# Kernel tuning notes

Hardware: AMD Instinct MI355X
Metric: run time of the kernel (lower is better)

## Reference

```python
import jax, jax.numpy as jnp
import numpy as np

T, B, D, H, L = 512, 64, 1024, 1024, 2
W_SCALE = 0.02  # keep tanh out of saturation


def setup_inputs() -> dict:
    key = jax.random.key(0)
    ks = jax.random.split(key, 7)
    return {
        "x": jax.random.normal(ks[0], (T, B, D), dtype=jnp.float32),
        "Wi": jax.random.normal(ks[1], (L, H, D), dtype=jnp.float32) * W_SCALE,
        "bi": jax.random.normal(ks[2], (L, H), dtype=jnp.float32) * W_SCALE,
        "Wh": jax.random.normal(ks[3], (L, H, H), dtype=jnp.float32) * W_SCALE,
        "bh": jax.random.normal(ks[4], (L, H), dtype=jnp.float32) * W_SCALE,
        "Wo": jax.random.normal(ks[5], (L, H, H), dtype=jnp.float32) * W_SCALE,
        "bo": jax.random.normal(ks[6], (L, H), dtype=jnp.float32) * W_SCALE,
    }


def reference(x, Wi, bi, Wh, bh, Wo, bo):
    # Faithful to the original: ONE hidden state shared across all layers,
    # overwritten by each RNNCell call within a timestep.
    num_layers = Wi.shape[0]
    batch = x.shape[1]
    hidden0 = jnp.zeros((batch, Wh.shape[-1]), dtype=x.dtype)

    def step(hidden, xt):
        out = xt
        for l in range(num_layers):
            # h = i2h(out) + h2h(hidden); o = h2o(h); new hidden = tanh(h)
            h = out @ Wi[l].T + bi[l] + hidden @ Wh[l].T + bh[l]  # [B,H]
            out = h @ Wo[l].T + bo[l]
            hidden = jnp.tanh(h)
        return hidden, out

    final_hidden, outs = jax.lax.scan(step, hidden0, x)  # outs: [T,B,H]
    return outs, final_hidden
```

## Files before the change

### kernel.cpp

```cpp
#include <hip/hip_runtime.h>
#include <cstdint>
#include <cstddef>

#define TT   512
#define NWG  256
#define SLOT 65536
#define FINALOFF ((size_t)TT * (size_t)SLOT)

#define OFF_M     0
#define OFF_H0    2097152
#define OFF_TH0   (OFF_H0 + 131072)
#define OFF_H1    (OFF_TH0 + 131072)
#define OFF_TH1   (OFF_H1 + 131072)
#define OFF_B0    (OFF_TH1 + 131072)
#define OFF_C1    (OFF_B0 + 4096)
#define OFF_FLAGS (OFF_C1 + 4096)

typedef _Float16 f16;
typedef unsigned long long ull;
typedef _Float16 v8h __attribute__((ext_vector_type(8)));
typedef float v4f __attribute__((ext_vector_type(4)));

union U2 { ull u[2]; v8h v; };

__device__ __forceinline__ void st8(void* p, ull v) {
  __hip_atomic_store((ull*)p, v, __ATOMIC_RELAXED, __HIP_MEMORY_SCOPE_AGENT);
}
__device__ __forceinline__ ull ld8(const void* p) {
  return __hip_atomic_load((const ull*)p, __ATOMIC_RELAXED, __HIP_MEMORY_SCOPE_AGENT);
}

__device__ __forceinline__ float rcpf(float x) {
#if __has_builtin(__builtin_amdgcn_rcpf)
  return __builtin_amdgcn_rcpf(x);
#else
  return 1.0f / x;
#endif
}
__device__ __forceinline__ float tanhfast(float x) {
  x = fminf(fmaxf(x, -20.0f), 20.0f);
  const float u = __expf(-2.0f * x);
  return 1.0f - 2.0f * u * rcpf(1.0f + u);
}

__global__ void k_init(unsigned int* flags) {
  flags[threadIdx.x] = 0u;
}

__global__ void k_bias(const float* __restrict__ Wi, const float* __restrict__ bi,
                       const float* __restrict__ bh, const float* __restrict__ bo,
                       float* __restrict__ b0, float* __restrict__ c1) {
  const int i = blockIdx.x * 256 + threadIdx.x;
  const float* row = Wi + 1048576 + (size_t)i * 1024;
  float s = 0.f;
  for (int k = 0; k < 1024; k += 4) {
    const float4 w = *(const float4*)&row[k];
    const float4 v = *(const float4*)&bo[k];
    s += w.x * v.x + w.y * v.y + w.z * v.z + w.w * v.w;
  }
  c1[i] = s + bi[1024 + i] + bh[1024 + i];
  b0[i] = bi[i] + bh[i];
}

__global__ __launch_bounds__(256) void k_gemm_M(const float* __restrict__ Wi,
                                                const float* __restrict__ Wo,
                                                f16* __restrict__ Mh) {
  const float* A = Wi + 1048576;
  const float* B = Wo;
  __shared__ float As[16][68];
  __shared__ float Bs[16][68];
  const int bi = blockIdx.x >> 4, bj = blockIdx.x & 15;
  const int i0 = bi * 64, d0 = bj * 64;
  const int ti = threadIdx.x >> 4, tj = threadIdx.x & 15;
  float acc[4][4] = {};
  for (int kc = 0; kc < 1024; kc += 16) {
    const int r = threadIdx.x >> 2, cg = (threadIdx.x & 3) << 2;
    const float4 av = *(const float4*)&A[(size_t)(i0 + r) * 1024 + kc + cg];
    As[cg + 0][r] = av.x; As[cg + 1][r] = av.y; As[cg + 2][r] = av.z; As[cg + 3][r] = av.w;
    const int c2 = threadIdx.x >> 4, dg = (threadIdx.x & 15) << 2;
    const float4 bv = *(const float4*)&B[(size_t)(kc + c2) * 1024 + d0 + dg];
    *(float4*)&Bs[c2][dg] = bv;
    __syncthreads();
#pragma unroll
    for (int kk = 0; kk < 16; ++kk) {
      float a[4], b[4];
#pragma unroll
      for (int q = 0; q < 4; ++q) { a[q] = As[kk][ti * 4 + q]; b[q] = Bs[kk][tj * 4 + q]; }
#pragma unroll
      for (int p = 0; p < 4; ++p)
#pragma unroll
        for (int q = 0; q < 4; ++q) acc[p][q] += a[p] * b[q];
    }
    __syncthreads();
  }
#pragma unroll
  for (int p = 0; p < 4; ++p)
#pragma unroll
    for (int q = 0; q < 4; ++q)
      Mh[(size_t)(i0 + ti * 4 + p) * 1024 + (size_t)(d0 + tj * 4 + q)] = (f16)acc[p][q];
}

__device__ __forceinline__ void gbar_arrive(unsigned int* gf, int slot, unsigned int ph) {
  asm volatile("s_waitcnt vmcnt(0)" ::: "memory");
  __syncthreads();
  if (threadIdx.x == 0)
    __hip_atomic_store(&gf[slot * 4], ph, __ATOMIC_RELAXED, __HIP_MEMORY_SCOPE_AGENT);
}
__device__ __forceinline__ void gbar_wait(unsigned int* gf, unsigned int ph) {
  if (threadIdx.x < 64)
    while (__hip_atomic_load(&gf[threadIdx.x * 4], __ATOMIC_RELAXED, __HIP_MEMORY_SCOPE_AGENT) < ph)
      __builtin_amdgcn_s_sleep(1);
  __syncthreads();
  asm volatile("" ::: "memory");
}

__device__ __forceinline__ void ld_frags(const f16* base, v8h out[8]) {
  ull u0[8], u1[8];
#pragma unroll
  for (int s = 0; s < 8; ++s) { const f16* p = base + s * 32; u0[s] = ld8(p); u1[s] = ld8(p + 4); }
#pragma unroll
  for (int s = 0; s < 8; ++s) { U2 c; c.u[0] = u0[s]; c.u[1] = u1[s]; out[s] = c.v; }
}

__global__ __launch_bounds__(256, 1) void k_rnn(
    const float* __restrict__ x,
    const float* __restrict__ Wi, const float* __restrict__ Wh,
    const float* __restrict__ Wo, const float* __restrict__ bo,
    char* __restrict__ ws, float* __restrict__ dout)
{
  const f16* Mh  = (const f16*)(ws + OFF_M);
  f16* h0h  = (f16*)(ws + OFF_H0);
  f16* th0h = (f16*)(ws + OFF_TH0);
  f16* h1h  = (f16*)(ws + OFF_H1);
  f16* th1h = (f16*)(ws + OFF_TH1);
  const float* b0p = (const float*)(ws + OFF_B0);
  const float* c1p = (const float*)(ws + OFF_C1);
  unsigned int* flags = (unsigned int*)(ws + OFF_FLAGS);

  const int wg = blockIdx.x;
  const int bq = wg & 3;
  const int jt = wg >> 2;
  const int j0 = jt * 16;
  const int tid = threadIdx.x;
  const int l = tid & 63, w = tid >> 6;
  const int lj = l & 15, lk = l >> 4;
  const int jrow = j0 + lj;
  unsigned int* gf = flags + bq * 256;

  __shared__ __align__(16) f16 WiL[16 * 1032];
  __shared__ float red[1024];
  __shared__ f16 trh[256];
  __shared__ f16 trh2[256];
  __shared__ float trf[256];

  v8h wWh0[8], wM[8], wWh1[8], wWo1[8];
#pragma unroll
  for (int s = 0; s < 8; ++s) {
    const int k0 = w * 256 + s * 32 + lk * 8;
    {
      const float* p = &Wh[(size_t)jrow * 1024 + k0];
      float4 a = *(const float4*)p, b = *(const float4*)(p + 4);
      wWh0[s] = (v8h){(f16)a.x,(f16)a.y,(f16)a.z,(f16)a.w,(f16)b.x,(f16)b.y,(f16)b.z,(f16)b.w};
    }
    {
      const float* p = &Wh[1048576 + (size_t)jrow * 1024 + k0];
      float4 a = *(const float4*)p, b = *(const float4*)(p + 4);
      wWh1[s] = (v8h){(f16)a.x,(f16)a.y,(f16)a.z,(f16)a.w,(f16)b.x,(f16)b.y,(f16)b.z,(f16)b.w};
    }
    {
      const float* p = &Wo[1048576 + (size_t)jrow * 1024 + k0];
      float4 a = *(const float4*)p, b = *(const float4*)(p + 4);
      wWo1[s] = (v8h){(f16)a.x,(f16)a.y,(f16)a.z,(f16)a.w,(f16)b.x,(f16)b.y,(f16)b.z,(f16)b.w};
    }
    wM[s] = *(const v8h*)&Mh[(size_t)jrow * 1024 + k0];
  }
  for (int u = tid; u < 4096; u += 256) {
    const int rr = u >> 8, c4 = (u & 255) << 2;
    const float4 v = *(const float4*)&Wi[(size_t)(j0 + rr) * 1024 + c4];
    f16* dst = &WiL[rr * 1032 + c4];
    dst[0] = (f16)v.x; dst[1] = (f16)v.y; dst[2] = (f16)v.z; dst[3] = (f16)v.w;
  }
  const int rj = tid & 15;
  const float b0v = b0p[j0 + rj];
  const float c1v = c1p[j0 + rj];
  const float bo1v = bo[1024 + j0 + rj];
  __syncthreads();

  const size_t actbase = (size_t)(bq * 16 + lj) * 1024 + (size_t)(w * 256 + lk * 8);
  const int redw = w * 256 + lk * 64 + lj;

  auto z1_dot = [&](const float* xt) -> float {
    v4f acc = {0.f, 0.f, 0.f, 0.f};
#pragma unroll
    for (int s = 0; s < 8; ++s) {
      const float* p = xt + actbase + s * 32;
      const float4 a = *(const float4*)p;
      const float4 b = *(const float4*)(p + 4);
      const v8h af = {(f16)a.x,(f16)a.y,(f16)a.z,(f16)a.w,
                      (f16)b.x,(f16)b.y,(f16)b.z,(f16)b.w};
      const v8h bf = *(const v8h*)&WiL[lj * 1032 + w * 256 + s * 32 + lk * 8];
      acc = __builtin_amdgcn_mfma_f32_16x16x32_f16(af, bf, acc, 0, 0, 0);
    }
#pragma unroll
    for (int q = 0; q < 4; ++q) red[redw + q * 16] = acc[q];
    __syncthreads();
    const float r = red[tid] + red[256 + tid] + red[512 + tid] + red[768 + tid] + b0v;
    __syncthreads();
    return r;
  };

  float zc = z1_dot(x);
  unsigned int ph = 0;

  for (int t = 0; t <= TT; ++t) {
    const bool A = (t < TT), R = (t > 0);
    v8h thf[8], hrf[8];

    if (R) {
      ld_frags(th1h + actbase, thf);
      ld_frags(h1h + actbase, hrf);
    }

    {
      v4f acc = {0.f, 0.f, 0.f, 0.f};
      if (R) {
#pragma unroll
        for (int s = 0; s < 8; ++s)
          acc = __builtin_amdgcn_mfma_f32_16x16x32_f16(thf[s], wWh0[s], acc, 0, 0, 0);
      }
#pragma unroll
      for (int q = 0; q < 4; ++q) red[redw + q * 16] = acc[q];
      __syncthreads();
      if (A) {
        const float h0 = red[tid] + red[256 + tid] + red[512 + tid] + red[768 + tid] + zc;
        trh[tid] = (f16)h0;
        trh2[tid] = (f16)tanhfast(h0);
      }
      __syncthreads();
      if (A) {
        if (tid < 64) {
          st8(&h0h[(size_t)(bq * 16 + (tid >> 2)) * 1024 + j0 + (tid & 3) * 4],
              ((const ull*)trh)[tid]);
        } else if (tid < 128) {
          const int u = tid - 64;
          st8(&th0h[(size_t)(bq * 16 + (u >> 2)) * 1024 + j0 + (u & 3) * 4],
              ((const ull*)trh2)[u]);
        }
      }
    }
    gbar_arrive(gf, jt, ++ph);

    if (R) {
      v4f a2 = {0.f, 0.f, 0.f, 0.f};
#pragma unroll
      for (int s = 0; s < 8; ++s)
        a2 = __builtin_amdgcn_mfma_f32_16x16x32_f16(hrf[s], wWo1[s], a2, 0, 0, 0);
#pragma unroll
      for (int q = 0; q < 4; ++q) red[redw + q * 16] = a2[q];
      __syncthreads();
      trf[tid] = red[tid] + red[256 + tid] + red[512 + tid] + red[768 + tid] + bo1v;
      __syncthreads();
      if (tid < 128)
        st8(&dout[(size_t)(t - 1) * SLOT + (size_t)(bq * 16 + (tid >> 3)) * 1024 + j0 + (tid & 7) * 2],
            ((const ull*)trf)[tid]);
    }
    gbar_wait(gf, ph);

    if (A) {
      v8h g0f[8], t0f[8];
      ld_frags(h0h + actbase, g0f);
      ld_frags(th0h + actbase, t0f);
      v4f aM = {0.f, 0.f, 0.f, 0.f}, aW = {0.f, 0.f, 0.f, 0.f};
#pragma unroll
      for (int s = 0; s < 8; ++s) {
        aM = __builtin_amdgcn_mfma_f32_16x16x32_f16(g0f[s], wM[s], aM, 0, 0, 0);
        aW = __builtin_amdgcn_mfma_f32_16x16x32_f16(t0f[s], wWh1[s], aW, 0, 0, 0);
      }
#pragma unroll
      for (int q = 0; q < 4; ++q) red[redw + q * 16] = aM[q] + aW[q];
      __syncthreads();
      const float h1 = red[tid] + red[256 + tid] + red[512 + tid] + red[768 + tid] + c1v;
      const bool last = (t == TT - 1);
      trh[tid] = (f16)h1;
      const float th1v = tanhfast(h1);
      trh2[tid] = (f16)th1v;
      if (last) trf[tid] = th1v;
      __syncthreads();
      if (tid < 64) {
        st8(&h1h[(size_t)(bq * 16 + (tid >> 2)) * 1024 + j0 + (tid & 3) * 4],
            ((const ull*)trh)[tid]);
      } else if (tid < 128) {
        const int u = tid - 64;
        st8(&th1h[(size_t)(bq * 16 + (u >> 2)) * 1024 + j0 + (u & 3) * 4],
            ((const ull*)trh2)[u]);
      }
      if (last && tid < 128)
        st8(&dout[FINALOFF + (size_t)(bq * 16 + (tid >> 3)) * 1024 + j0 + (tid & 7) * 2],
            ((const ull*)trf)[tid]);
      gbar_arrive(gf, jt, ++ph);

      float zn = zc;
      if (t + 1 < TT)
        zn = z1_dot(x + (size_t)(t + 1) * SLOT);
      gbar_wait(gf, ph);
      zc = zn;
    }
  }
}

extern "C" void kernel_launch(void* const* d_in, const int* in_sizes, int n_in,
                              void* d_out, int out_size, void* d_ws, size_t ws_size,
                              hipStream_t stream) {
  (void)in_sizes; (void)n_in; (void)out_size; (void)ws_size;
  const float* x  = (const float*)d_in[0];
  const float* Wi = (const float*)d_in[1];
  const float* bi = (const float*)d_in[2];
  const float* Wh = (const float*)d_in[3];
  const float* bh = (const float*)d_in[4];
  const float* Wo = (const float*)d_in[5];
  const float* bo = (const float*)d_in[6];
  char* ws = (char*)d_ws;
  float* out = (float*)d_out;

  k_init<<<1, 1024, 0, stream>>>((unsigned int*)(ws + OFF_FLAGS));
  k_bias<<<4, 256, 0, stream>>>(Wi, bi, bh, bo, (float*)(ws + OFF_B0), (float*)(ws + OFF_C1));
  k_gemm_M<<<256, 256, 0, stream>>>(Wi, Wo, (f16*)(ws + OFF_M));
  k_rnn<<<NWG, 256, 0, stream>>>(x, Wi, Wh, Wo, bo, ws, out);
}
```

Before: 6.767 ms.

## Split RNN into critical-path and auxiliary workgroups with separate barrier flags

Doubles the persistent grid to 512 workgroups. 256 critical workgroups run only the recurrent h0/h1 chain. 256 auxiliary workgroups compute the input projection z (double-buffered two steps ahead) and the per-step output projection, using their own flag array. This takes the Wo GEMV, the output stores and the x projection off the serial recurrence so they overlap with it. In exchange, h1 is double-buffered, stores become 2-byte atomics instead of packed 8-byte ones, and two workgroups must share a CU, since launch bounds now allow 2 per CU. Spin-wait co-residency becomes a deadlock risk if all 512 workgroups are not resident at once.

```diff
diff --git a/kernel.cpp b/kernel.cpp
--- a/kernel.cpp
+++ b/kernel.cpp
@@ -3,18 +3,22 @@
 #include <cstddef>
 
 #define TT   512
-#define NWG  256
+#define NWG  512
 #define SLOT 65536
 #define FINALOFF ((size_t)TT * (size_t)SLOT)
 
 #define OFF_M     0
 #define OFF_H0    2097152
 #define OFF_TH0   (OFF_H0 + 131072)
-#define OFF_H1    (OFF_TH0 + 131072)
-#define OFF_TH1   (OFF_H1 + 131072)
-#define OFF_B0    (OFF_TH1 + 131072)
+#define OFF_H1A   (OFF_TH0 + 131072)
+#define OFF_H1B   (OFF_H1A + 131072)
+#define OFF_TH1   (OFF_H1B + 131072)
+#define OFF_Z0    (OFF_TH1 + 131072)
+#define OFF_Z1    (OFF_Z0 + 131072)
+#define OFF_B0    (OFF_Z1 + 131072)
 #define OFF_C1    (OFF_B0 + 4096)
-#define OFF_FLAGS (OFF_C1 + 4096)
+#define OFF_CF    (OFF_C1 + 4096)
+#define OFF_AF    (OFF_CF + 4096)
 
 typedef _Float16 f16;
 typedef unsigned long long ull;
@@ -23,8 +27,14 @@
 
 union U2 { ull u[2]; v8h v; };
 
-__device__ __forceinline__ void st8(void* p, ull v) {
-  __hip_atomic_store((ull*)p, v, __ATOMIC_RELAXED, __HIP_MEMORY_SCOPE_AGENT);
+__device__ __forceinline__ void st2(void* p, f16 v) {
+  __hip_atomic_store((unsigned short*)p, __builtin_bit_cast(unsigned short, v),
+                     __ATOMIC_RELAXED, __HIP_MEMORY_SCOPE_AGENT);
+}
+__device__ __forceinline__ f16 ld2(const void* p) {
+  unsigned short u = __hip_atomic_load((const unsigned short*)p,
+                                       __ATOMIC_RELAXED, __HIP_MEMORY_SCOPE_AGENT);
+  return __builtin_bit_cast(f16, u);
 }
 __device__ __forceinline__ ull ld8(const void* p) {
   return __hip_atomic_load((const ull*)p, __ATOMIC_RELAXED, __HIP_MEMORY_SCOPE_AGENT);
@@ -44,7 +54,7 @@
 }
 
 __global__ void k_init(unsigned int* flags) {
-  flags[threadIdx.x] = 0u;
+  flags[blockIdx.x * 1024 + threadIdx.x] = 0u;
 }
 
 __global__ void k_bias(const float* __restrict__ Wi, const float* __restrict__ bi,
@@ -100,20 +110,6 @@
       Mh[(size_t)(i0 + ti * 4 + p) * 1024 + (size_t)(d0 + tj * 4 + q)] = (f16)acc[p][q];
 }
 
-__device__ __forceinline__ void gbar_arrive(unsigned int* gf, int slot, unsigned int ph) {
-  asm volatile("s_waitcnt vmcnt(0)" ::: "memory");
-  __syncthreads();
-  if (threadIdx.x == 0)
-    __hip_atomic_store(&gf[slot * 4], ph, __ATOMIC_RELAXED, __HIP_MEMORY_SCOPE_AGENT);
-}
-__device__ __forceinline__ void gbar_wait(unsigned int* gf, unsigned int ph) {
-  if (threadIdx.x < 64)
-    while (__hip_atomic_load(&gf[threadIdx.x * 4], __ATOMIC_RELAXED, __HIP_MEMORY_SCOPE_AGENT) < ph)
-      __builtin_amdgcn_s_sleep(1);
-  __syncthreads();
-  asm volatile("" ::: "memory");
-}
-
 __device__ __forceinline__ void ld_frags(const f16* base, v8h out[8]) {
   ull u0[8], u1[8];
 #pragma unroll
@@ -122,7 +118,7 @@
   for (int s = 0; s < 8; ++s) { U2 c; c.u[0] = u0[s]; c.u[1] = u1[s]; out[s] = c.v; }
 }
 
-__global__ __launch_bounds__(256, 1) void k_rnn(
+__global__ __launch_bounds__(256, 2) void k_rnn(
     const float* __restrict__ x,
     const float* __restrict__ Wi, const float* __restrict__ Wh,
     const float* __restrict__ Wo, const float* __restrict__ bo,
@@ -131,99 +127,70 @@
   const f16* Mh  = (const f16*)(ws + OFF_M);
   f16* h0h  = (f16*)(ws + OFF_H0);
   f16* th0h = (f16*)(ws + OFF_TH0);
-  f16* h1h  = (f16*)(ws + OFF_H1);
+  f16* h1b[2] = { (f16*)(ws + OFF_H1A), (f16*)(ws + OFF_H1B) };
   f16* th1h = (f16*)(ws + OFF_TH1);
+  f16* zb[2] = { (f16*)(ws + OFF_Z0), (f16*)(ws + OFF_Z1) };
   const float* b0p = (const float*)(ws + OFF_B0);
   const float* c1p = (const float*)(ws + OFF_C1);
-  unsigned int* flags = (unsigned int*)(ws + OFF_FLAGS);
 
   const int wg = blockIdx.x;
-  const int bq = wg & 3;
-  const int jt = wg >> 2;
+  const bool is_aux = (wg >= 256);
+  const int p = is_aux ? (wg - 256) : wg;
+  const int bq = p & 3;
+  const int jt = p >> 2;
   const int j0 = jt * 16;
   const int tid = threadIdx.x;
   const int l = tid & 63, w = tid >> 6;
   const int lj = l & 15, lk = l >> 4;
   const int jrow = j0 + lj;
-  unsigned int* gf = flags + bq * 256;
+  const int rb = tid >> 4, rj = tid & 15;
+
+  unsigned int* gfC = (unsigned int*)(ws + OFF_CF) + bq * 256;
+  unsigned int* gfA = (unsigned int*)(ws + OFF_AF) + bq * 256;
 
   __shared__ __align__(16) f16 WiL[16 * 1032];
   __shared__ float red[1024];
-  __shared__ f16 trh[256];
-  __shared__ f16 trh2[256];
-  __shared__ float trf[256];
-
-  v8h wWh0[8], wM[8], wWh1[8], wWo1[8];
-#pragma unroll
-  for (int s = 0; s < 8; ++s) {
-    const int k0 = w * 256 + s * 32 + lk * 8;
-    {
-      const float* p = &Wh[(size_t)jrow * 1024 + k0];
-      float4 a = *(const float4*)p, b = *(const float4*)(p + 4);
-      wWh0[s] = (v8h){(f16)a.x,(f16)a.y,(f16)a.z,(f16)a.w,(f16)b.x,(f16)b.y,(f16)b.z,(f16)b.w};
-    }
-    {
-      const float* p = &Wh[1048576 + (size_t)jrow * 1024 + k0];
-      float4 a = *(const float4*)p, b = *(const float4*)(p + 4);
-      wWh1[s] = (v8h){(f16)a.x,(f16)a.y,(f16)a.z,(f16)a.w,(f16)b.x,(f16)b.y,(f16)b.z,(f16)b.w};
-    }
-    {
-      const float* p = &Wo[1048576 + (size_t)jrow * 1024 + k0];
-      float4 a = *(const float4*)p, b = *(const float4*)(p + 4);
-      wWo1[s] = (v8h){(f16)a.x,(f16)a.y,(f16)a.z,(f16)a.w,(f16)b.x,(f16)b.y,(f16)b.z,(f16)b.w};
-    }
-    wM[s] = *(const v8h*)&Mh[(size_t)jrow * 1024 + k0];
-  }
-  for (int u = tid; u < 4096; u += 256) {
-    const int rr = u >> 8, c4 = (u & 255) << 2;
-    const float4 v = *(const float4*)&Wi[(size_t)(j0 + rr) * 1024 + c4];
-    f16* dst = &WiL[rr * 1032 + c4];
-    dst[0] = (f16)v.x; dst[1] = (f16)v.y; dst[2] = (f16)v.z; dst[3] = (f16)v.w;
-  }
-  const int rj = tid & 15;
-  const float b0v = b0p[j0 + rj];
-  const float c1v = c1p[j0 + rj];
-  const float bo1v = bo[1024 + j0 + rj];
-  __syncthreads();
 
   const size_t actbase = (size_t)(bq * 16 + lj) * 1024 + (size_t)(w * 256 + lk * 8);
   const int redw = w * 256 + lk * 64 + lj;
-
-  auto z1_dot = [&](const float* xt) -> float {
-    v4f acc = {0.f, 0.f, 0.f, 0.f};
+  const size_t rdst = (size_t)(bq * 16 + rb) * 1024 + (size_t)(j0 + rj);
+
+  if (!is_aux) {
+    v8h wWh0[8], wM[8], wWh1[8];
 #pragma unroll
     for (int s = 0; s < 8; ++s) {
-      const float* p = xt + actbase + s * 32;
-      const float4 a = *(const float4*)p;
-      const float4 b = *(const float4*)(p + 4);
-      const v8h af = {(f16)a.x,(f16)a.y,(f16)a.z,(f16)a.w,
-                      (f16)b.x,(f16)b.y,(f16)b.z,(f16)b.w};
-      const v8h bf = *(const v8h*)&WiL[lj * 1032 + w * 256 + s * 32 + lk * 8];
-      acc = __builtin_amdgcn_mfma_f32_16x16x32_f16(af, bf, acc, 0, 0, 0);
-    }
-#pragma unroll
-    for (int q = 0; q < 4; ++q) red[redw + q * 16] = acc[q];
-    __syncthreads();
-    const float r = red[tid] + red[256 + tid] + red[512 + tid] + red[768 + tid] + b0v;
-    __syncthreads();
-    return r;
-  };
-
-  float zc = z1_dot(x);
-  unsigned int ph = 0;
-
-  for (int t = 0; t <= TT; ++t) {
-    const bool A = (t < TT), R = (t > 0);
-    v8h thf[8], hrf[8];
-
-    if (R) {
-      ld_frags(th1h + actbase, thf);
-      ld_frags(h1h + actbase, hrf);
-    }
-
-    {
+      const int k0 = w * 256 + s * 32 + lk * 8;
+      {
+        const float* pp = &Wh[(size_t)jrow * 1024 + k0];
+        float4 a = *(const float4*)pp, b = *(const float4*)(pp + 4);
+        wWh0[s] = (v8h){(f16)a.x,(f16)a.y,(f16)a.z,(f16)a.w,(f16)b.x,(f16)b.y,(f16)b.z,(f16)b.w};
+      }
+      {
+        const float* pp = &Wh[1048576 + (size_t)jrow * 1024 + k0];
+        float4 a = *(const float4*)pp, b = *(const float4*)(pp + 4);
+        wWh1[s] = (v8h){(f16)a.x,(f16)a.y,(f16)a.z,(f16)a.w,(f16)b.x,(f16)b.y,(f16)b.z,(f16)b.w};
+      }
+      wM[s] = *(const v8h*)&Mh[(size_t)jrow * 1024 + k0];
+    }
+    const float c1v = c1p[j0 + rj];
+
+    for (int t = 0; t < TT; ++t) {
+      const unsigned int cthA = 2u * t;
+      const unsigned int athA = (t == 0) ? 1u : (unsigned int)t;
+      if (tid < 64) {
+        while (__hip_atomic_load(&gfC[tid * 4], __ATOMIC_RELAXED, __HIP_MEMORY_SCOPE_AGENT) < cthA)
+          __builtin_amdgcn_s_sleep(1);
+      } else if (tid < 128) {
+        while (__hip_atomic_load(&gfA[(tid - 64) * 4], __ATOMIC_RELAXED, __HIP_MEMORY_SCOPE_AGENT) < athA)
+          __builtin_amdgcn_s_sleep(1);
+      }
+      __syncthreads();
+
+      const f16 zv = ld2(&zb[t & 1][rdst]);
       v4f acc = {0.f, 0.f, 0.f, 0.f};
-      if (R) {
+      if (t > 0) {
+        v8h thf[8];
+        ld_frags(th1h + actbase, thf);
 #pragma unroll
         for (int s = 0; s < 8; ++s)
           acc = __builtin_amdgcn_mfma_f32_16x16x32_f16(thf[s], wWh0[s], acc, 0, 0, 0);
@@ -231,42 +198,20 @@
 #pragma unroll
       for (int q = 0; q < 4; ++q) red[redw + q * 16] = acc[q];
       __syncthreads();
-      if (A) {
-        const float h0 = red[tid] + red[256 + tid] + red[512 + tid] + red[768 + tid] + zc;
-        trh[tid] = (f16)h0;
-        trh2[tid] = (f16)tanhfast(h0);
-      }
-      __syncthreads();
-      if (A) {
-        if (tid < 64) {
-          st8(&h0h[(size_t)(bq * 16 + (tid >> 2)) * 1024 + j0 + (tid & 3) * 4],
-              ((const ull*)trh)[tid]);
-        } else if (tid < 128) {
-          const int u = tid - 64;
-          st8(&th0h[(size_t)(bq * 16 + (u >> 2)) * 1024 + j0 + (u & 3) * 4],
-              ((const ull*)trh2)[u]);
-        }
-      }
-    }
-    gbar_arrive(gf, jt, ++ph);
-
-    if (R) {
-      v4f a2 = {0.f, 0.f, 0.f, 0.f};
-#pragma unroll
-      for (int s = 0; s < 8; ++s)
-        a2 = __builtin_amdgcn_mfma_f32_16x16x32_f16(hrf[s], wWo1[s], a2, 0, 0, 0);
-#pragma unroll
-      for (int q = 0; q < 4; ++q) red[redw + q * 16] = a2[q];
-      __syncthreads();
-      trf[tid] = red[tid] + red[256 + tid] + red[512 + tid] + red[768 + tid] + bo1v;
-      __syncthreads();
-      if (tid < 128)
-        st8(&dout[(size_t)(t - 1) * SLOT + (size_t)(bq * 16 + (tid >> 3)) * 1024 + j0 + (tid & 7) * 2],
-            ((const ull*)trf)[tid]);
-    }
-    gbar_wait(gf, ph);
-
-    if (A) {
+      const float h0 = red[tid] + red[256 + tid] + red[512 + tid] + red[768 + tid] + (float)zv;
+      st2(&h0h[rdst], (f16)h0);
+      st2(&th0h[rdst], (f16)tanhfast(h0));
+      asm volatile("s_waitcnt vmcnt(0)" ::: "memory");
+      __syncthreads();
+      if (tid == 0)
+        __hip_atomic_store(&gfC[jt * 4], 2u * t + 1u, __ATOMIC_RELAXED, __HIP_MEMORY_SCOPE_AGENT);
+
+      if (tid < 64) {
+        while (__hip_atomic_load(&gfC[tid * 4], __ATOMIC_RELAXED, __HIP_MEMORY_SCOPE_AGENT) < 2u * t + 1u)
+          __builtin_amdgcn_s_sleep(1);
+      }
+      __syncthreads();
+
       v8h g0f[8], t0f[8];
       ld_frags(h0h + actbase, g0f);
       ld_frags(th0h + actbase, t0f);
@@ -280,30 +225,86 @@
       for (int q = 0; q < 4; ++q) red[redw + q * 16] = aM[q] + aW[q];
       __syncthreads();
       const float h1 = red[tid] + red[256 + tid] + red[512 + tid] + red[768 + tid] + c1v;
-      const bool last = (t == TT - 1);
-      trh[tid] = (f16)h1;
       const float th1v = tanhfast(h1);
-      trh2[tid] = (f16)th1v;
-      if (last) trf[tid] = th1v;
-      __syncthreads();
+      st2(&h1b[t & 1][rdst], (f16)h1);
+      st2(&th1h[rdst], (f16)th1v);
+      if (t == TT - 1) dout[FINALOFF + rdst] = th1v;
+      asm volatile("s_waitcnt vmcnt(0)" ::: "memory");
+      __syncthreads();
+      if (tid == 0)
+        __hip_atomic_store(&gfC[jt * 4], 2u * t + 2u, __ATOMIC_RELAXED, __HIP_MEMORY_SCOPE_AGENT);
+    }
+  } else {
+    v8h wWo1[8];
+#pragma unroll
+    for (int s = 0; s < 8; ++s) {
+      const int k0 = w * 256 + s * 32 + lk * 8;
+      const float* pp = &Wo[1048576 + (size_t)jrow * 1024 + k0];
+      float4 a = *(const float4*)pp, b = *(const float4*)(pp + 4);
+      wWo1[s] = (v8h){(f16)a.x,(f16)a.y,(f16)a.z,(f16)a.w,(f16)b.x,(f16)b.y,(f16)b.z,(f16)b.w};
+    }
+    for (int u = tid; u < 4096; u += 256) {
+      const int rr = u >> 8, c4 = (u & 255) << 2;
+      const float4 v = *(const float4*)&Wi[(size_t)(j0 + rr) * 1024 + c4];
+      f16* dst = &WiL[rr * 1032 + c4];
+      dst[0] = (f16)v.x; dst[1] = (f16)v.y; dst[2] = (f16)v.z; dst[3] = (f16)v.w;
+    }
+    const float b0v = b0p[j0 + rj];
+    const float bo1v = bo[1024 + j0 + rj];
+    __syncthreads();
+
+    auto z1c = [&](const float* xt, f16* zdst) {
+      __syncthreads();
+      v4f acc = {0.f, 0.f, 0.f, 0.f};
+#pragma unroll
+      for (int s = 0; s < 8; ++s) {
+        const float* pp = xt + actbase + s * 32;
+        const float4 a = *(const float4*)pp;
+        const float4 b = *(const float4*)(pp + 4);
+        const v8h af = {(f16)a.x,(f16)a.y,(f16)a.z,(f16)a.w,
+                        (f16)b.x,(f16)b.y,(f16)b.z,(f16)b.w};
+        const v8h bf = *(const v8h*)&WiL[lj * 1032 + w * 256 + s * 32 + lk * 8];
+        acc = __builtin_amdgcn_mfma_f32_16x16x32_f16(af, bf, acc, 0, 0, 0);
+      }
+#pragma unroll
+      for (int q = 0; q < 4; ++q) red[redw + q * 16] = acc[q];
+      __syncthreads();
+      const float r = red[tid] + red[256 + tid] + red[512 + tid] + red[768 + tid] + b0v;
+      st2(&zdst[rdst], (f16)r);
+    };
+
+    z1c(x, zb[0]);
+    z1c(x + SLOT, zb[1]);
+    asm volatile("s_waitcnt vmcnt(0)" ::: "memory");
+    __syncthreads();
+    if (tid == 0)
+      __hip_atomic_store(&gfA[jt * 4], 1u, __ATOMIC_RELAXED, __HIP_MEMORY_SCOPE_AGENT);
+
+    for (int i = 1; i <= TT; ++i) {
       if (tid < 64) {
-        st8(&h1h[(size_t)(bq * 16 + (tid >> 2)) * 1024 + j0 + (tid & 3) * 4],
-            ((const ull*)trh)[tid]);
-      } else if (tid < 128) {
-        const int u = tid - 64;
-        st8(&th1h[(size_t)(bq * 16 + (u >> 2)) * 1024 + j0 + (u & 3) * 4],
-            ((const ull*)trh2)[u]);
-      }
-      if (last && tid < 128)
-        st8(&dout[FINALOFF + (size_t)(bq * 16 + (tid >> 3)) * 1024 + j0 + (tid & 7) * 2],
-            ((const ull*)trf)[tid]);
-      gbar_arrive(gf, jt, ++ph);
-
-      float zn = zc;
-      if (t + 1 < TT)
-        zn = z1_dot(x + (size_t)(t + 1) * SLOT);
-      gbar_wait(gf, ph);
-      zc = zn;
+        while (__hip_atomic_load(&gfC[tid * 4], __ATOMIC_RELAXED, __HIP_MEMORY_SCOPE_AGENT) < 2u * i)
+          __builtin_amdgcn_s_sleep(1);
+      }
+      __syncthreads();
+
+      v8h hrf[8];
+      ld_frags(h1b[(i - 1) & 1] + actbase, hrf);
+      v4f a2 = {0.f, 0.f, 0.f, 0.f};
+#pragma unroll
+      for (int s = 0; s < 8; ++s)
+        a2 = __builtin_amdgcn_mfma_f32_16x16x32_f16(hrf[s], wWo1[s], a2, 0, 0, 0);
+#pragma unroll
+      for (int q = 0; q < 4; ++q) red[redw + q * 16] = a2[q];
+      __syncthreads();
+      const float s1 = red[tid] + red[256 + tid] + red[512 + tid] + red[768 + tid] + bo1v;
+      dout[(size_t)(i - 1) * SLOT + rdst] = s1;
+
+      if (i + 1 < TT) z1c(x + (size_t)(i + 1) * SLOT, zb[(i + 1) & 1]);
+
+      asm volatile("s_waitcnt vmcnt(0)" ::: "memory");
+      __syncthreads();
+      if (tid == 0)
+        __hip_atomic_store(&gfA[jt * 4], (unsigned int)(i + 1), __ATOMIC_RELAXED, __HIP_MEMORY_SCOPE_AGENT);
     }
   }
 }
@@ -322,7 +323,7 @@
   char* ws = (char*)d_ws;
   float* out = (float*)d_out;
 
-  k_init<<<1, 1024, 0, stream>>>((unsigned int*)(ws + OFF_FLAGS));
+  k_init<<<2, 1024, 0, stream>>>((unsigned int*)(ws + OFF_CF));
   k_bias<<<4, 256, 0, stream>>>(Wi, bi, bh, bo, (float*)(ws + OFF_B0), (float*)(ws + OFF_C1));
   k_gemm_M<<<256, 256, 0, stream>>>(Wi, Wo, (f16*)(ws + OFF_M));
   k_rnn<<<NWG, 256, 0, stream>>>(x, Wi, Wh, Wo, bo, ws, out);
```

Measured after the change: 6.437 ms. 1.05x faster.
